# Optimization experiments

Measured on AMD Instinct MI355X. Metric: run time of the kernel, lower is better.

Reference implementation:

```python
import jax, jax.numpy as jnp
from jax import lax
import numpy as np

GRID = 64
HIDDEN = 256
FEAT = 128


def setup_inputs() -> dict:
    key = jax.random.key(0)
    ks = jax.random.split(key, 16)
    B, S = 1024, 4096
    def w(k, shape, fan_in):
        return (jax.random.normal(k, shape, jnp.float32) * (1.0 / np.sqrt(fan_in))).astype(jnp.float32)
    return {
        "x": jax.random.normal(ks[0], (B, 2, S), jnp.float32),
        # conv stack
        "w1": w(ks[1], (32, 1, 3, 3), 9),    "b1": jnp.zeros((32,), jnp.float32),  "a1": jnp.float32(0.25),
        "w2": w(ks[2], (64, 32, 3, 3), 32 * 9),  "b2": jnp.zeros((64,), jnp.float32),  "a2": jnp.float32(0.25),
        "w3": w(ks[3], (128, 64, 5, 5), 64 * 25), "b3": jnp.zeros((128,), jnp.float32), "a3": jnp.float32(0.25),
        # classifier (dropout is identity in eval mode)
        "wc1": w(ks[4], (HIDDEN, 128 * 4 * 4), 128 * 16), "bc1": jnp.zeros((HIDDEN,), jnp.float32), "ac": jnp.float32(0.25),
        "wc2": w(ks[5], (FEAT, HIDDEN), HIDDEN),          "bc2": jnp.zeros((FEAT,), jnp.float32),
    }


def _prelu(x, a):
    return jnp.where(x > 0, x, a * x)


def _conv(x, w, b, pad):
    y = lax.conv_general_dilated(x, w, (1, 1), [(pad, pad), (pad, pad)],
                                 dimension_numbers=("NCHW", "OIHW", "NCHW"))
    return y + b[None, :, None, None]


def _avgpool2(x):  # kernel 2, stride 2 (also serves as adaptive pool 8->4)
    B, C, H, W = x.shape
    return x.reshape(B, C, H // 2, 2, W // 2, 2).mean(axis=(3, 5))


def _iq_to_constellation(x):
    # x: [B, 2, S] -> occupancy grid [B, 1, G, G] (set to 1.0, duplicates collapse)
    B = x.shape[0]
    scale = GRID // 2 / 2.0
    offset = GRID // 2
    ii = jnp.clip((x[:, 0] * scale + offset).astype(jnp.int32), 0, GRID - 1)  # [B,S]
    qi = jnp.clip((x[:, 1] * scale + offset).astype(jnp.int32), 0, GRID - 1)
    img = jnp.zeros((B, 1, GRID, GRID), x.dtype)
    bidx = jnp.arange(B)[:, None]
    return img.at[bidx, 0, qi, ii].set(1.0)


def reference(x, w1, b1, a1, w2, b2, a2, w3, b3, a3, wc1, bc1, ac, wc2, bc2):
    img = _iq_to_constellation(x)                      # [B,1,64,64]
    h = _avgpool2(_prelu(_conv(img, w1, b1, 1), a1))   # [B,32,32,32]
    h = _avgpool2(_prelu(_conv(h, w2, b2, 1), a2))     # [B,64,16,16]
    h = _avgpool2(_prelu(_conv(h, w3, b3, 2), a3))     # [B,128,8,8]
    h = _avgpool2(h)                                   # adaptive 8x8 -> 4x4
    h = h.reshape(h.shape[0], -1)                      # [B, 2048]
    h = _prelu(h @ wc1.T + bc1, ac)                    # [B, 256]
    return h @ wc2.T + bc2                             # [B, 128]
```

## Files before the change

### kernel.cpp

```cpp
#include <hip/hip_runtime.h>


typedef short s16x8 __attribute__((ext_vector_type(8)));
typedef float f32x4 __attribute__((ext_vector_type(4)));
typedef unsigned u32x4 __attribute__((ext_vector_type(4)));
typedef unsigned u32x2 __attribute__((ext_vector_type(2)));

__device__ __forceinline__ float prelu(float v, float a) {
    return v > 0.0f ? v : a * v;
}
__device__ __forceinline__ unsigned short bf16_rn(float x) {
    union { float f; unsigned u; } a; a.f = x;
    unsigned r = a.u + 0x7FFF + ((a.u >> 16) & 1);
    return (unsigned short)(r >> 16);
}
__device__ __forceinline__ unsigned pack2(float lo, float hi) {
    return (unsigned)bf16_rn(lo) | ((unsigned)bf16_rn(hi) << 16);
}

__global__ __launch_bounds__(256) void k_prepack3(
    const float* __restrict__ w3, unsigned short* __restrict__ wpk)
{
    int e = blockIdx.x * 256 + threadIdx.x;
    int i  = e & 7;
    int co = (e >> 3) & 127;
    int g  = (e >> 10) & 3;
    int kk = (e >> 12) & 1;
    int tp = e >> 13;
    int ci = kk * 32 + g * 8 + i;
    wpk[e] = bf16_rn(w3[((size_t)co * 64 + ci) * 25 + tp]);
}

__global__ __launch_bounds__(256) void k_prepack2(
    const float* __restrict__ w2, unsigned short* __restrict__ wpk)
{
    int e = blockIdx.x * 256 + threadIdx.x;
    int i  = e & 7;
    int co = (e >> 3) & 63;
    int g  = (e >> 9) & 3;
    int tp = e >> 11;
    int ci = g * 8 + i;
    wpk[e] = bf16_rn(w2[((size_t)co * 32 + ci) * 9 + tp]);
}

__global__ __launch_bounds__(256) void k_prepack_fc1(
    const float* __restrict__ wc1, unsigned short* __restrict__ wpk)
{
    int e = blockIdx.x * 256 + threadIdx.x;
    int i   = e & 7;
    int hid = (e >> 3) & 255;
    int g   = (e >> 11) & 3;
    int kc  = e >> 13;
    int k = kc * 32 + g * 8 + i;
    wpk[e] = bf16_rn(wc1[(size_t)hid * 2048 + k]);
}

__global__ __launch_bounds__(256) void k_prepack_fc2(
    const float* __restrict__ wc2, unsigned short* __restrict__ wpk)
{
    int e = blockIdx.x * 256 + threadIdx.x;
    int i  = e & 7;
    int o  = (e >> 3) & 127;
    int g  = (e >> 10) & 3;
    int kc = e >> 12;
    int k = kc * 32 + g * 8 + i;
    wpk[e] = bf16_rn(wc2[(size_t)o * 256 + k]);
}

__global__ __launch_bounds__(256) void k_scat_conv1(
    const float* __restrict__ x, const float* __restrict__ w1,
    const float* __restrict__ b1, const float* __restrict__ a1,
    unsigned short* __restrict__ out1, int b0)
{
    __shared__ float img[34 * 66];
    __shared__ float ws[32 * 9];
    __shared__ float bs[32];
    const int t = threadIdx.x;
    const int bl = blockIdx.x >> 1;
    const int yb = blockIdx.x & 1;
    const int b = b0 + bl;

    for (int i = t; i < 34 * 66; i += 256) img[i] = 0.0f;
    for (int i = t; i < 288; i += 256) ws[i] = w1[i];
    if (t < 32) bs[t] = b1[t];
    __syncthreads();

    const float* xb = x + (size_t)b * 8192;
    const int rbase = yb * 32 - 1;
    for (int s = t; s < 4096; s += 256) {
        float xi = xb[s];
        float xq = xb[4096 + s];
        int ii = (int)(xi * 16.0f + 32.0f);
        int qi = (int)(xq * 16.0f + 32.0f);
        ii = min(max(ii, 0), 63);
        qi = min(max(qi, 0), 63);
        int r = qi - rbase;
        if (r >= 0 && r < 34) img[r * 66 + (ii + 1)] = 1.0f;
    }
    __syncthreads();

    const float alpha = a1[0];
    unsigned short* ob = out1 + (size_t)bl * 32768;
    for (int i = 0; i < 2; ++i) {
        int p = i * 256 + t;
        int pyl = p >> 5, px = p & 31;
        float v[4][4];
        #pragma unroll
        for (int r = 0; r < 4; ++r)
            #pragma unroll
            for (int c = 0; c < 4; ++c)
                v[r][c] = img[(2 * pyl + r) * 66 + (2 * px + c)];
        const int pg = (yb * 16 + pyl) * 32 + px;
        unsigned short* dst = ob + (size_t)pg * 32;
        #pragma unroll 2
        for (int c4 = 0; c4 < 8; ++c4) {
            float o4[4];
            #pragma unroll
            for (int h = 0; h < 4; ++h) {
                const int c = c4 * 4 + h;
                float w[9];
                #pragma unroll
                for (int k = 0; k < 9; ++k) w[k] = ws[c * 9 + k];
                float s00 = 0.f, s01 = 0.f, s10 = 0.f, s11 = 0.f;
                #pragma unroll
                for (int ky = 0; ky < 3; ++ky)
                    #pragma unroll
                    for (int kx = 0; kx < 3; ++kx) {
                        float wk = w[ky * 3 + kx];
                        s00 = fmaf(v[ky][kx],         wk, s00);
                        s01 = fmaf(v[ky][kx + 1],     wk, s01);
                        s10 = fmaf(v[ky + 1][kx],     wk, s10);
                        s11 = fmaf(v[ky + 1][kx + 1], wk, s11);
                    }
                float bb = bs[c];
                o4[h] = 0.25f * (prelu(s00 + bb, alpha) + prelu(s01 + bb, alpha) +
                                 prelu(s10 + bb, alpha) + prelu(s11 + bb, alpha));
            }
            u32x2 q = {pack2(o4[0], o4[1]), pack2(o4[2], o4[3])};
            *reinterpret_cast<u32x2*>(dst + c4 * 4) = q;
        }
    }
}

__global__ __launch_bounds__(512) void k_conv2_mfma(
    const unsigned short* __restrict__ in1, const unsigned short* __restrict__ wpk,
    const float* __restrict__ b2, const float* __restrict__ a2,
    unsigned short* __restrict__ out2)
{
    __shared__ __align__(16) unsigned short lb[4 * 18 * 36 * 8];
    __shared__ float bs[64];
    const int t = threadIdx.x;
    const int bl = blockIdx.x >> 1;
    const int yb = blockIdx.x & 1;
    const int lane = t & 63;
    const int w = t >> 6;
    const int mp = w >> 2;
    const int nq = w & 3;
    const int lg = lane >> 4;
    const int lo16 = lane & 15;

    if (t < 64) bs[t] = b2[t];

    const f32x4 zf = {0.f, 0.f, 0.f, 0.f};
    f32x4 acc[2][8];
    #pragma unroll
    for (int m = 0; m < 2; ++m)
        #pragma unroll
        for (int n = 0; n < 8; ++n) acc[m][n] = zf;

    const s16x8 zz = {0, 0, 0, 0, 0, 0, 0, 0};
    for (int idx = t; idx < 2592; idx += 512)
        reinterpret_cast<s16x8*>(lb)[idx] = zz;
    __syncthreads();

    for (int idx = t; idx < 576; idx += 512) {
        int ly = idx >> 5;
        int xx = idx & 31;
        int y = yb * 16 + ly - 1;
        if (y >= 0 && y < 32) {
            const s16x8* src = reinterpret_cast<const s16x8*>(
                in1 + ((size_t)bl * 1024 + y * 32 + xx) * 32);
            #pragma unroll
            for (int cg = 0; cg < 4; ++cg) {
                *reinterpret_cast<s16x8*>(&lb[((cg * 18 + ly) * 36 + (xx + 1)) * 8]) = src[cg];
            }
        }
    }
    __syncthreads();

    #pragma unroll
    for (int tap = 0; tap < 9; ++tap) {
        const int dy = tap / 3, dx = tap - dy * 3;
        const size_t wbase = ((size_t)tap * 4 + lg) * 512 + (size_t)(mp * 32 + lo16) * 8;
        s16x8 a0 = *reinterpret_cast<const s16x8*>(wpk + wbase);
        s16x8 a1 = *reinterpret_cast<const s16x8*>(wpk + wbase + 128);
        #pragma unroll
        for (int n = 0; n < 8; ++n) {
            const int rl = n >> 1, xh = n & 1;
            const int ly = nq * 4 + rl + dy;
            const int sx = xh * 16 + lo16 + dx;
            s16x8 bfrag = *reinterpret_cast<const s16x8*>(
                &lb[((lg * 18 + ly) * 36 + sx) * 8]);
            acc[0][n] = __builtin_amdgcn_mfma_f32_16x16x32_bf16(a0, bfrag, acc[0][n], 0, 0, 0);
            acc[1][n] = __builtin_amdgcn_mfma_f32_16x16x32_bf16(a1, bfrag, acc[1][n], 0, 0, 0);
        }
    }

    const float alpha = a2[0];
    #pragma unroll
    for (int m = 0; m < 2; ++m) {
        const int co = mp * 32 + m * 16 + lg * 4;
        #pragma unroll
        for (int pr = 0; pr < 2; ++pr) {
            #pragma unroll
            for (int xh = 0; xh < 2; ++xh) {
                float sr[4];
                #pragma unroll
                for (int r = 0; r < 4; ++r) {
                    const float bb = bs[co + r];
                    float v0 = acc[m][(pr * 2) * 2 + xh][r] + bb;
                    float v1 = acc[m][(pr * 2 + 1) * 2 + xh][r] + bb;
                    float s = prelu(v0, alpha) + prelu(v1, alpha);
                    s += __shfl_xor(s, 1, 64);
                    sr[r] = s * 0.25f;
                }
                if (!(lo16 & 1)) {
                    int gy = yb * 8 + nq * 2 + pr;
                    int gx = xh * 8 + (lo16 >> 1);
                    u32x2 q = {pack2(sr[0], sr[1]), pack2(sr[2], sr[3])};
                    *reinterpret_cast<u32x2*>(
                        out2 + ((size_t)bl * 256 + gy * 16 + gx) * 64 + co) = q;
                }
            }
        }
    }
}

__global__ __launch_bounds__(512) void k_conv3_mfma(
    const unsigned short* __restrict__ in2, const unsigned short* __restrict__ wpk,
    const float* __restrict__ b3, const float* __restrict__ a3,
    unsigned short* __restrict__ out3h, int b0)
{
    __shared__ __align__(16) unsigned short lb[8 * 20 * 20 * 8];
    __shared__ float bs[128];

    const int t = threadIdx.x;
    const int bl = blockIdx.x;
    const int lane = t & 63;
    const int w = t >> 6;
    const int mp = w >> 1;
    const int nh = w & 1;
    const int lg = lane >> 4;
    const int lo16 = lane & 15;

    if (t < 128) bs[t] = b3[t];

    const s16x8 zz = {0, 0, 0, 0, 0, 0, 0, 0};
    for (int idx = t; idx < 3200; idx += 512)
        reinterpret_cast<s16x8*>(lb)[idx] = zz;
    __syncthreads();

    for (int idx = t; idx < 2048; idx += 512) {
        int g = idx >> 8;
        int pix = idx & 255;
        int row = pix >> 4;
        int xx = pix & 15;
        s16x8 v = *reinterpret_cast<const s16x8*>(
            in2 + ((size_t)bl * 256 + row * 16 + xx) * 64 + g * 8);
        *reinterpret_cast<s16x8*>(&lb[((g * 20 + (row + 2)) * 20 + (xx + 2)) * 8]) = v;
    }
    __syncthreads();

    const f32x4 zf = {0.f, 0.f, 0.f, 0.f};
    f32x4 acc[2][8];
    #pragma unroll
    for (int m = 0; m < 2; ++m)
        #pragma unroll
        for (int n = 0; n < 8; ++n) acc[m][n] = zf;

    for (int kk = 0; kk < 2; ++kk) {
        for (int tap = 0; tap < 25; ++tap) {
            int dy = tap / 5, dx = tap - dy * 5;
            const size_t wbase = ((size_t)(tap * 2 + kk) * 4 + lg) * 1024
                               + (size_t)(mp * 32 + lo16) * 8;
            s16x8 a0 = *reinterpret_cast<const s16x8*>(wpk + wbase);
            s16x8 a1 = *reinterpret_cast<const s16x8*>(wpk + wbase + 128);
            #pragma unroll
            for (int n = 0; n < 8; ++n) {
                int ly = nh * 8 + n + dy;
                int ax = lo16 + dx;
                s16x8 bfrag = *reinterpret_cast<const s16x8*>(
                    &lb[(((kk * 4 + lg) * 20 + ly) * 20 + ax) * 8]);
                acc[0][n] = __builtin_amdgcn_mfma_f32_16x16x32_bf16(a0, bfrag, acc[0][n], 0, 0, 0);
                acc[1][n] = __builtin_amdgcn_mfma_f32_16x16x32_bf16(a1, bfrag, acc[1][n], 0, 0, 0);
            }
        }
    }

    const float alpha = a3[0];
    const int b = b0 + bl;
    const int fx = lo16 >> 2;
    #pragma unroll
    for (int m = 0; m < 2; ++m) {
        const int cobase = mp * 32 + m * 16 + lg * 4;
        #pragma unroll
        for (int r = 0; r < 4; ++r) {
            float bb = bs[cobase + r];
            #pragma unroll
            for (int half = 0; half < 2; ++half) {
                float s = 0.f;
                #pragma unroll
                for (int j = 0; j < 4; ++j) {
                    float v = acc[m][half * 4 + j][r] + bb;
                    s += v > 0.f ? v : alpha * v;
                }
                s += __shfl_xor(s, 1, 64);
                s += __shfl_xor(s, 2, 64);
                if ((lane & 3) == 0) {
                    int fy = nh * 2 + half;
                    out3h[(size_t)b * 2048 + (cobase + r) * 16 + fy * 4 + fx] =
                        bf16_rn(s * 0.0625f);
                }
            }
        }
    }
}

__global__ __launch_bounds__(512) void k_fc_mfma(
    const unsigned short* __restrict__ h, const unsigned short* __restrict__ w1pk,
    const float* __restrict__ bc1, const float* __restrict__ ac,
    const unsigned short* __restrict__ w2pk, const float* __restrict__ bc2,
    float* __restrict__ out)
{
    __shared__ __align__(16) unsigned short hid_lds[32][264];
    __shared__ float bs1[256];
    __shared__ float bs2[128];
    const int t = threadIdx.x;
    const int lane = t & 63;
    const int w = t >> 6;
    const int nl = w & 1;
    const int mq = w >> 1;
    const int lg = lane >> 4;
    const int lo16 = lane & 15;

    if (t < 256) bs1[t] = bc1[t];
    if (t < 128) bs2[t] = bc2[t];

    const int b_local = nl * 16 + lo16;
    const size_t rb = (size_t)blockIdx.x * 32 + b_local;

    const f32x4 zf = {0.f, 0.f, 0.f, 0.f};
    f32x4 acc1[4];
    #pragma unroll
    for (int mt = 0; mt < 4; ++mt) acc1[mt] = zf;

    const unsigned short* hrow = h + rb * 2048;
    #pragma unroll 2
    for (int kc = 0; kc < 64; ++kc) {
        s16x8 bfrag = *reinterpret_cast<const s16x8*>(hrow + kc * 32 + lg * 8);
        #pragma unroll
        for (int mt = 0; mt < 4; ++mt) {
            s16x8 afr = *reinterpret_cast<const s16x8*>(
                w1pk + ((size_t)(kc * 4 + lg) * 256 + (mq * 4 + mt) * 16 + lo16) * 8);
            acc1[mt] = __builtin_amdgcn_mfma_f32_16x16x32_bf16(afr, bfrag, acc1[mt], 0, 0, 0);
        }
    }

    __syncthreads();
    const float alpha = ac[0];
    #pragma unroll
    for (int mt = 0; mt < 4; ++mt) {
        const int hid0 = (mq * 4 + mt) * 16 + lg * 4;
        float v0 = prelu(acc1[mt][0] + bs1[hid0 + 0], alpha);
        float v1 = prelu(acc1[mt][1] + bs1[hid0 + 1], alpha);
        float v2 = prelu(acc1[mt][2] + bs1[hid0 + 2], alpha);
        float v3 = prelu(acc1[mt][3] + bs1[hid0 + 3], alpha);
        u32x2 q = {pack2(v0, v1), pack2(v2, v3)};
        *reinterpret_cast<u32x2*>(&hid_lds[b_local][hid0]) = q;
    }
    __syncthreads();

    f32x4 acc2[2];
    acc2[0] = zf; acc2[1] = zf;
    #pragma unroll
    for (int kc = 0; kc < 8; ++kc) {
        s16x8 bfrag = *reinterpret_cast<const s16x8*>(&hid_lds[b_local][kc * 32 + lg * 8]);
        #pragma unroll
        for (int mt = 0; mt < 2; ++mt) {
            s16x8 afr = *reinterpret_cast<const s16x8*>(
                w2pk + ((size_t)(kc * 4 + lg) * 128 + (mq * 2 + mt) * 16 + lo16) * 8);
            acc2[mt] = __builtin_amdgcn_mfma_f32_16x16x32_bf16(afr, bfrag, acc2[mt], 0, 0, 0);
        }
    }

    #pragma unroll
    for (int mt = 0; mt < 2; ++mt) {
        const int o0 = (mq * 2 + mt) * 16 + lg * 4;
        #pragma unroll
        for (int r = 0; r < 4; ++r)
            out[rb * 128 + o0 + r] = acc2[mt][r] + bs2[o0 + r];
    }
}

extern "C" void kernel_launch(void* const* d_in, const int* in_sizes, int n_in,
                              void* d_out, int out_size, void* d_ws, size_t ws_size,
                              hipStream_t stream) {
    const float* x   = (const float*)d_in[0];
    const float* w1  = (const float*)d_in[1];
    const float* b1  = (const float*)d_in[2];
    const float* a1  = (const float*)d_in[3];
    const float* w2  = (const float*)d_in[4];
    const float* b2  = (const float*)d_in[5];
    const float* a2  = (const float*)d_in[6];
    const float* w3  = (const float*)d_in[7];
    const float* b3  = (const float*)d_in[8];
    const float* a3  = (const float*)d_in[9];
    const float* wc1 = (const float*)d_in[10];
    const float* bc1 = (const float*)d_in[11];
    const float* ac  = (const float*)d_in[12];
    const float* wc2 = (const float*)d_in[13];
    const float* bc2 = (const float*)d_in[14];
    float* out = (float*)d_out;

    const size_t OUT3_BYTES = (size_t)1024 * 2048 * 2;
    const size_t W3PK = (size_t)204800 * 2;
    const size_t W2PK = (size_t)18432 * 2;
    const size_t WFC1 = (size_t)524288 * 2;
    const size_t WFC2 = (size_t)32768 * 2;
    const size_t FIXED = OUT3_BYTES + W3PK + W2PK + WFC1 + WFC2;
    int C = 1024;
    while (C > 1 && FIXED + (size_t)C * (65536 + 32768) > ws_size) C >>= 1;

    char* p = (char*)d_ws;
    unsigned short* out3h = (unsigned short*)p;  p += OUT3_BYTES;
    unsigned short* w3pk  = (unsigned short*)p;  p += W3PK;
    unsigned short* w2pk  = (unsigned short*)p;  p += W2PK;
    unsigned short* wf1pk = (unsigned short*)p;  p += WFC1;
    unsigned short* wf2pk = (unsigned short*)p;  p += WFC2;
    unsigned short* out1  = (unsigned short*)p;  p += (size_t)C * 65536;
    unsigned short* out2  = (unsigned short*)p;

    k_prepack3<<<800, 256, 0, stream>>>(w3, w3pk);
    k_prepack2<<<72, 256, 0, stream>>>(w2, w2pk);
    k_prepack_fc1<<<2048, 256, 0, stream>>>(wc1, wf1pk);
    k_prepack_fc2<<<128, 256, 0, stream>>>(wc2, wf2pk);

    const int nchunk = 1024 / C;
    for (int c = 0; c < nchunk; ++c) {
        int b0 = c * C;
        k_scat_conv1<<<2 * C, 256, 0, stream>>>(x, w1, b1, a1, out1, b0);
        k_conv2_mfma<<<2 * C, 512, 0, stream>>>(out1, w2pk, b2, a2, out2);
        k_conv3_mfma<<<C, 512, 0, stream>>>(out2, w3pk, b3, a3, out3h, b0);
    }
    k_fc_mfma<<<32, 512, 0, stream>>>(out3h, wf1pk, bc1, ac, wf2pk, bc2, out);
}
```

Measured before the change: 256.0 us.

## Switch conv2 and conv3 to 32x32x16 MFMA with repacked weights

Measured after the change: 293.2 us. 1.15x slower.

```diff
diff --git a/kernel.cpp b/kernel.cpp
--- a/kernel.cpp
+++ b/kernel.cpp
@@ -3,6 +3,7 @@
 
 typedef short s16x8 __attribute__((ext_vector_type(8)));
 typedef float f32x4 __attribute__((ext_vector_type(4)));
+typedef float f32x16 __attribute__((ext_vector_type(16)));
 typedef unsigned u32x4 __attribute__((ext_vector_type(4)));
 typedef unsigned u32x2 __attribute__((ext_vector_type(2)));
 
@@ -22,25 +23,28 @@
     const float* __restrict__ w3, unsigned short* __restrict__ wpk)
 {
     int e = blockIdx.x * 256 + threadIdx.x;
-    int i  = e & 7;
-    int co = (e >> 3) & 127;
-    int g  = (e >> 10) & 3;
-    int kk = (e >> 12) & 1;
-    int tp = e >> 13;
-    int ci = kk * 32 + g * 8 + i;
-    wpk[e] = bf16_rn(w3[((size_t)co * 64 + ci) * 25 + tp]);
+    int i   = e & 7;
+    int l   = (e >> 3) & 63;
+    int mt  = (e >> 9) & 3;
+    int kkk = (e >> 11) & 3;
+    int tap = e >> 13;
+    int co = mt * 32 + (l & 31);
+    int ci = kkk * 16 + (l >> 5) * 8 + i;
+    wpk[e] = bf16_rn(w3[((size_t)co * 64 + ci) * 25 + tap]);
 }
 
 __global__ __launch_bounds__(256) void k_prepack2(
     const float* __restrict__ w2, unsigned short* __restrict__ wpk)
 {
     int e = blockIdx.x * 256 + threadIdx.x;
-    int i  = e & 7;
-    int co = (e >> 3) & 63;
-    int g  = (e >> 9) & 3;
-    int tp = e >> 11;
-    int ci = g * 8 + i;
-    wpk[e] = bf16_rn(w2[((size_t)co * 32 + ci) * 9 + tp]);
+    int i   = e & 7;
+    int l   = (e >> 3) & 63;
+    int mt  = (e >> 9) & 1;
+    int kkk = (e >> 10) & 1;
+    int tap = e >> 11;
+    int co = mt * 32 + (l & 31);
+    int ci = kkk * 16 + (l >> 5) * 8 + i;
+    wpk[e] = bf16_rn(w2[((size_t)co * 32 + ci) * 9 + tap]);
 }
 
 __global__ __launch_bounds__(256) void k_prepack_fc1(
@@ -153,20 +157,11 @@
     const int bl = blockIdx.x >> 1;
     const int yb = blockIdx.x & 1;
     const int lane = t & 63;
-    const int w = t >> 6;
-    const int mp = w >> 2;
-    const int nq = w & 3;
-    const int lg = lane >> 4;
-    const int lo16 = lane & 15;
+    const int q = t >> 6;
+    const int hl = lane >> 5;
+    const int c31 = lane & 31;
 
     if (t < 64) bs[t] = b2[t];
-
-    const f32x4 zf = {0.f, 0.f, 0.f, 0.f};
-    f32x4 acc[2][8];
-    #pragma unroll
-    for (int m = 0; m < 2; ++m)
-        #pragma unroll
-        for (int n = 0; n < 8; ++n) acc[m][n] = zf;
 
     const s16x8 zz = {0, 0, 0, 0, 0, 0, 0, 0};
     for (int idx = t; idx < 2592; idx += 512)
@@ -188,49 +183,59 @@
     }
     __syncthreads();
 
-    #pragma unroll
-    for (int tap = 0; tap < 9; ++tap) {
-        const int dy = tap / 3, dx = tap - dy * 3;
-        const size_t wbase = ((size_t)tap * 4 + lg) * 512 + (size_t)(mp * 32 + lo16) * 8;
-        s16x8 a0 = *reinterpret_cast<const s16x8*>(wpk + wbase);
-        s16x8 a1 = *reinterpret_cast<const s16x8*>(wpk + wbase + 128);
-        #pragma unroll
-        for (int n = 0; n < 8; ++n) {
-            const int rl = n >> 1, xh = n & 1;
-            const int ly = nq * 4 + rl + dy;
-            const int sx = xh * 16 + lo16 + dx;
-            s16x8 bfrag = *reinterpret_cast<const s16x8*>(
-                &lb[((lg * 18 + ly) * 36 + sx) * 8]);
-            acc[0][n] = __builtin_amdgcn_mfma_f32_16x16x32_bf16(a0, bfrag, acc[0][n], 0, 0, 0);
-            acc[1][n] = __builtin_amdgcn_mfma_f32_16x16x32_bf16(a1, bfrag, acc[1][n], 0, 0, 0);
+    f32x16 acc[2][2];
+    #pragma unroll
+    for (int m = 0; m < 2; ++m)
+        #pragma unroll
+        for (int n = 0; n < 2; ++n)
+            #pragma unroll
+            for (int e = 0; e < 16; ++e) acc[m][n][e] = 0.0f;
+
+    for (int dy = 0; dy < 3; ++dy) {
+        for (int dx = 0; dx < 3; ++dx) {
+            const int tap = dy * 3 + dx;
+            #pragma unroll
+            for (int kkk = 0; kkk < 2; ++kkk) {
+                const unsigned short* wb =
+                    wpk + ((size_t)(tap * 2 + kkk) * 2) * 512 + lane * 8;
+                s16x8 a0 = *reinterpret_cast<const s16x8*>(wb);
+                s16x8 a1 = *reinterpret_cast<const s16x8*>(wb + 512);
+                const int g = kkk * 2 + hl;
+                const int r0 = 2 * q + dy;
+                const int sx = c31 + dx;
+                s16x8 bf0 = *reinterpret_cast<const s16x8*>(
+                    &lb[((g * 18 + r0) * 36 + sx) * 8]);
+                s16x8 bf1 = *reinterpret_cast<const s16x8*>(
+                    &lb[((g * 18 + r0 + 1) * 36 + sx) * 8]);
+                acc[0][0] = __builtin_amdgcn_mfma_f32_32x32x16_bf16(a0, bf0, acc[0][0], 0, 0, 0);
+                acc[0][1] = __builtin_amdgcn_mfma_f32_32x32x16_bf16(a0, bf1, acc[0][1], 0, 0, 0);
+                acc[1][0] = __builtin_amdgcn_mfma_f32_32x32x16_bf16(a1, bf0, acc[1][0], 0, 0, 0);
+                acc[1][1] = __builtin_amdgcn_mfma_f32_32x32x16_bf16(a1, bf1, acc[1][1], 0, 0, 0);
+            }
         }
     }
 
     const float alpha = a2[0];
-    #pragma unroll
-    for (int m = 0; m < 2; ++m) {
-        const int co = mp * 32 + m * 16 + lg * 4;
-        #pragma unroll
-        for (int pr = 0; pr < 2; ++pr) {
-            #pragma unroll
-            for (int xh = 0; xh < 2; ++xh) {
-                float sr[4];
-                #pragma unroll
-                for (int r = 0; r < 4; ++r) {
-                    const float bb = bs[co + r];
-                    float v0 = acc[m][(pr * 2) * 2 + xh][r] + bb;
-                    float v1 = acc[m][(pr * 2 + 1) * 2 + xh][r] + bb;
-                    float s = prelu(v0, alpha) + prelu(v1, alpha);
-                    s += __shfl_xor(s, 1, 64);
-                    sr[r] = s * 0.25f;
-                }
-                if (!(lo16 & 1)) {
-                    int gy = yb * 8 + nq * 2 + pr;
-                    int gx = xh * 8 + (lo16 >> 1);
-                    u32x2 q = {pack2(sr[0], sr[1]), pack2(sr[2], sr[3])};
-                    *reinterpret_cast<u32x2*>(
-                        out2 + ((size_t)bl * 256 + gy * 16 + gx) * 64 + co) = q;
-                }
+    const int gy = yb * 8 + q;
+    const int gx = c31 >> 1;
+    #pragma unroll
+    for (int mt = 0; mt < 2; ++mt) {
+        float sv[16];
+        #pragma unroll
+        for (int r = 0; r < 16; ++r) {
+            const int co = mt * 32 + (r & 3) + 8 * (r >> 2) + 4 * hl;
+            const float bb = bs[co];
+            float s = prelu(acc[mt][0][r] + bb, alpha) + prelu(acc[mt][1][r] + bb, alpha);
+            s += __shfl_xor(s, 1, 64);
+            sv[r] = s * 0.25f;
+        }
+        if ((lane & 1) == 0) {
+            unsigned short* dst = out2 + ((size_t)bl * 256 + gy * 16 + gx) * 64;
+            #pragma unroll
+            for (int rp = 0; rp < 8; ++rp) {
+                const int r = rp * 2;
+                const int co0 = mt * 32 + (r & 3) + 8 * (r >> 2) + 4 * hl;
+                *reinterpret_cast<unsigned*>(dst + co0) = pack2(sv[r], sv[r + 1]);
             }
         }
     }
@@ -248,10 +253,11 @@
     const int bl = blockIdx.x;
     const int lane = t & 63;
     const int w = t >> 6;
-    const int mp = w >> 1;
-    const int nh = w & 1;
-    const int lg = lane >> 4;
-    const int lo16 = lane & 15;
+    const int mg = w >> 2;
+    const int nq = w & 3;
+    const int hl = lane >> 5;
+    const int px = lane & 15;
+    const int ry = (lane >> 4) & 1;
 
     if (t < 128) bs[t] = b3[t];
 
@@ -271,57 +277,54 @@
     }
     __syncthreads();
 
-    const f32x4 zf = {0.f, 0.f, 0.f, 0.f};
-    f32x4 acc[2][8];
+    f32x16 acc[2][2];
     #pragma unroll
     for (int m = 0; m < 2; ++m)
         #pragma unroll
-        for (int n = 0; n < 8; ++n) acc[m][n] = zf;
-
-    for (int kk = 0; kk < 2; ++kk) {
-        for (int tap = 0; tap < 25; ++tap) {
-            int dy = tap / 5, dx = tap - dy * 5;
-            const size_t wbase = ((size_t)(tap * 2 + kk) * 4 + lg) * 1024
-                               + (size_t)(mp * 32 + lo16) * 8;
-            s16x8 a0 = *reinterpret_cast<const s16x8*>(wpk + wbase);
-            s16x8 a1 = *reinterpret_cast<const s16x8*>(wpk + wbase + 128);
-            #pragma unroll
-            for (int n = 0; n < 8; ++n) {
-                int ly = nh * 8 + n + dy;
-                int ax = lo16 + dx;
-                s16x8 bfrag = *reinterpret_cast<const s16x8*>(
-                    &lb[(((kk * 4 + lg) * 20 + ly) * 20 + ax) * 8]);
-                acc[0][n] = __builtin_amdgcn_mfma_f32_16x16x32_bf16(a0, bfrag, acc[0][n], 0, 0, 0);
-                acc[1][n] = __builtin_amdgcn_mfma_f32_16x16x32_bf16(a1, bfrag, acc[1][n], 0, 0, 0);
+        for (int n = 0; n < 2; ++n)
+            #pragma unroll
+            for (int e = 0; e < 16; ++e) acc[m][n][e] = 0.0f;
+
+    for (int dy = 0; dy < 5; ++dy) {
+        for (int dx = 0; dx < 5; ++dx) {
+            const int tap = dy * 5 + dx;
+            #pragma unroll
+            for (int kkk = 0; kkk < 4; ++kkk) {
+                const unsigned short* wb =
+                    wpk + ((size_t)(tap * 4 + kkk) * 4 + mg * 2) * 512 + lane * 8;
+                s16x8 a0 = *reinterpret_cast<const s16x8*>(wb);
+                s16x8 a1 = *reinterpret_cast<const s16x8*>(wb + 512);
+                const int g = kkk * 2 + hl;
+                const int r0 = 4 * nq + ry + dy;
+                const int ax = px + dx;
+                s16x8 bf0 = *reinterpret_cast<const s16x8*>(
+                    &lb[((g * 20 + r0) * 20 + ax) * 8]);
+                s16x8 bf1 = *reinterpret_cast<const s16x8*>(
+                    &lb[((g * 20 + r0 + 2) * 20 + ax) * 8]);
+                acc[0][0] = __builtin_amdgcn_mfma_f32_32x32x16_bf16(a0, bf0, acc[0][0], 0, 0, 0);
+                acc[0][1] = __builtin_amdgcn_mfma_f32_32x32x16_bf16(a0, bf1, acc[0][1], 0, 0, 0);
+                acc[1][0] = __builtin_amdgcn_mfma_f32_32x32x16_bf16(a1, bf0, acc[1][0], 0, 0, 0);
+                acc[1][1] = __builtin_amdgcn_mfma_f32_32x32x16_bf16(a1, bf1, acc[1][1], 0, 0, 0);
             }
         }
     }
 
     const float alpha = a3[0];
     const int b = b0 + bl;
-    const int fx = lo16 >> 2;
+    const int fx = px >> 2;
     #pragma unroll
     for (int m = 0; m < 2; ++m) {
-        const int cobase = mp * 32 + m * 16 + lg * 4;
-        #pragma unroll
-        for (int r = 0; r < 4; ++r) {
-            float bb = bs[cobase + r];
-            #pragma unroll
-            for (int half = 0; half < 2; ++half) {
-                float s = 0.f;
-                #pragma unroll
-                for (int j = 0; j < 4; ++j) {
-                    float v = acc[m][half * 4 + j][r] + bb;
-                    s += v > 0.f ? v : alpha * v;
-                }
-                s += __shfl_xor(s, 1, 64);
-                s += __shfl_xor(s, 2, 64);
-                if ((lane & 3) == 0) {
-                    int fy = nh * 2 + half;
-                    out3h[(size_t)b * 2048 + (cobase + r) * 16 + fy * 4 + fx] =
-                        bf16_rn(s * 0.0625f);
-                }
-            }
+        const int cb = (mg * 2 + m) * 32;
+        #pragma unroll
+        for (int r = 0; r < 16; ++r) {
+            const int co = cb + (r & 3) + 8 * (r >> 2) + 4 * hl;
+            const float bb = bs[co];
+            float s = prelu(acc[m][0][r] + bb, alpha) + prelu(acc[m][1][r] + bb, alpha);
+            s += __shfl_xor(s, 1, 64);
+            s += __shfl_xor(s, 2, 64);
+            s += __shfl_xor(s, 16, 64);
+            if ((lane & 19) == 0)
+                out3h[(size_t)b * 2048 + co * 16 + nq * 4 + fx] = bf16_rn(s * 0.0625f);
         }
     }
 }
```
